# Kernel tuning notes

Hardware: AMD Instinct MI355X
Metric: run time of the kernel (lower is better)

The kernel has to match this reference:

```python
import jax, jax.numpy as jnp
import numpy as np

N_NODES = 50000
N_EDGES = 400000
NODE_FEAT = 32
HIDDEN = 256
ACTION_DIM = 6
NUM_GRAPHS = 64


def setup_inputs() -> dict:
    key = jax.random.key(0)
    ks = jax.random.split(key, 9)
    x = jax.random.normal(ks[0], (N_NODES, NODE_FEAT), dtype=jnp.float32)
    edge_index = jax.random.randint(ks[1], (2, N_EDGES), 0, N_NODES, dtype=jnp.int32)
    batch = jnp.sort(jax.random.randint(ks[2], (N_NODES,), 0, NUM_GRAPHS, dtype=jnp.int32))
    # GCNConv weights (PyG stores Linear without bias + separate bias term;
    # here W is [in, out] so h = x @ W)
    s1 = 1.0 / np.sqrt(NODE_FEAT)
    s2 = 1.0 / np.sqrt(HIDDEN)
    W1 = jax.random.uniform(ks[3], (NODE_FEAT, HIDDEN), jnp.float32, -s1, s1)
    b1 = jnp.zeros((HIDDEN,), jnp.float32)
    W2 = jax.random.uniform(ks[4], (HIDDEN, HIDDEN), jnp.float32, -s2, s2)
    b2 = jnp.zeros((HIDDEN,), jnp.float32)
    Wf = jax.random.uniform(ks[5], (HIDDEN, 2 * ACTION_DIM), jnp.float32, -s2, s2)
    bf = jax.random.uniform(ks[6], (2 * ACTION_DIM,), jnp.float32, -s2, s2)
    return {"x": x, "edge_index": edge_index, "batch": batch,
            "W1": W1, "b1": b1, "W2": W2, "b2": b2, "Wf": Wf, "bf": bf}


def gcn_conv(x, src, dst, deg_inv_sqrt, W, b, num_nodes):
    # PyG GCNConv: h = x @ W, messages h[src] * norm scattered to dst, + bias.
    h = x @ W  # [N, out]
    norm = deg_inv_sqrt[src] * deg_inv_sqrt[dst]  # [E+N]
    msgs = h[src] * norm[:, None]  # [E+N, out]  (dominant memory traffic)
    out = jax.ops.segment_sum(msgs, dst, num_segments=num_nodes)
    return out + b


def reference(x, edge_index, batch, W1, b1, W2, b2, Wf, bf):
    num_nodes = x.shape[0]
    loop = jnp.arange(num_nodes, dtype=edge_index.dtype)
    src = jnp.concatenate([edge_index[0], loop])  # self-loops, PyG default
    dst = jnp.concatenate([edge_index[1], loop])
    deg = jax.ops.segment_sum(jnp.ones_like(dst, dtype=x.dtype), dst,
                              num_segments=num_nodes)  # >=1 due to self-loops
    deg_inv_sqrt = jax.lax.rsqrt(deg)

    h = jax.nn.relu(gcn_conv(x, src, dst, deg_inv_sqrt, W1, b1, num_nodes))
    h = jax.nn.relu(gcn_conv(h, src, dst, deg_inv_sqrt, W2, b2, num_nodes))

    # global_mean_pool over graph ids
    sums = jax.ops.segment_sum(h, batch, num_segments=NUM_GRAPHS)
    counts = jax.ops.segment_sum(jnp.ones((num_nodes,), x.dtype), batch,
                                 num_segments=NUM_GRAPHS)
    pooled = sums / jnp.maximum(counts, 1.0)[:, None]  # [G, HIDDEN]

    mls = pooled @ Wf + bf  # [G, 2*ACTION_DIM]
    mean, log_std = jnp.split(mls, 2, axis=-1)
    std = jnp.exp(jnp.clip(log_std, -20.0, 2.0))
    return mean, std
```

## Files before the change

### kernel.cpp

```cpp
#include <hip/hip_runtime.h>
#include <math.h>

#define NN 50000
#define FEAT 32
#define HID 256
#define NGRAPH 64
#define CAP 48

typedef __attribute__((ext_vector_type(8))) short bfrag;
typedef __attribute__((ext_vector_type(8))) unsigned short u16x8;
typedef __attribute__((ext_vector_type(4))) float f32x4;

__device__ __forceinline__ float bf2f(unsigned short u) {
    union { unsigned int i; float f; } v; v.i = ((unsigned int)u) << 16; return v.f;
}
__device__ __forceinline__ unsigned short f2bf(float f) {
    union { float f; unsigned int i; } v; v.f = f;
    unsigned int r = v.i + 0x7fffu + ((v.i >> 16) & 1u);
    return (unsigned short)(r >> 16);
}

__device__ __forceinline__ void pack_w(const float* __restrict__ W,
                                       unsigned short* __restrict__ Wp, int K, int o) {
    int j    = o & 7;
    int lane = (o >> 3) & 63;
    int rest = o >> 9;
    int nst  = K >> 5;
    int ks   = rest & (nst - 1);
    int nb   = rest / nst;
    int n = nb * 16 + (lane & 15);
    int k = ks * 32 + (lane >> 4) * 8 + j;
    Wp[o] = f2bf(W[(size_t)k * HID + n]);
}

__global__ void k_prep(float4* __restrict__ zp, int n16) {
    int i = blockIdx.x * blockDim.x + threadIdx.x;
    if (i < n16) zp[i] = make_float4(0.f, 0.f, 0.f, 0.f);
}

__global__ void k_setup(const int* __restrict__ src, const int* __restrict__ dst,
                        const int* __restrict__ batch,
                        const float* __restrict__ W1, const float* __restrict__ W2,
                        int* __restrict__ counter, unsigned short* __restrict__ csr,
                        int* __restrict__ starts, float* __restrict__ pooled,
                        unsigned short* __restrict__ W1p, unsigned short* __restrict__ W2p,
                        int E, int N) {
    int e = blockIdx.x * blockDim.x + threadIdx.x;
    if (e < E) {
        int d = dst[e];
        int p = atomicAdd(&counter[d], 1);
        if (p < CAP) csr[(size_t)d * CAP + p] = (unsigned short)src[e];
    }
    if (e < N) {
        int b = batch[e];
        int prev = (e == 0) ? -1 : batch[e - 1];
        if (b != prev) {
            for (int g = prev + 1; g <= b; ++g) starts[g] = e;
        }
        if (e == N - 1) {
            for (int g = b + 1; g <= NGRAPH; ++g) starts[g] = N;
        }
    }
    if (e < FEAT * HID) pack_w(W1, W1p, FEAT, e);
    int o2 = e - FEAT * HID;
    if (o2 >= 0 && o2 < HID * HID) pack_w(W2, W2p, HID, o2);
    if (e < NGRAPH * HID) pooled[e] = 0.f;
}

__global__ void k_aggx(const float* __restrict__ x, const int* __restrict__ cnt,
                       const unsigned short* __restrict__ csr,
                       unsigned short* __restrict__ out, int N) {
    int node = blockIdx.x * 8 + (threadIdx.x >> 5);
    if (node >= N) return;
    int col = threadIdx.x & 31;
    int ecnt = cnt[node];
    float dn = rsqrtf((float)(ecnt + 1));
    int e = ecnt > CAP ? CAP : ecnt;
    const unsigned short* lst = &csr[(size_t)node * CAP];

    float acc = x[(size_t)node * FEAT + col] * dn;
    int i = 0;
    for (; i + 8 <= e; i += 8) {
        u16x8 s = *(const u16x8*)&lst[i];
        float vs[8];
#pragma unroll
        for (int j = 0; j < 8; ++j) {
            int sj = (int)s[j];
            vs[j] = x[(size_t)sj * FEAT + col] * rsqrtf((float)(cnt[sj] + 1));
        }
        acc += ((vs[0] + vs[1]) + (vs[2] + vs[3])) + ((vs[4] + vs[5]) + (vs[6] + vs[7]));
    }
    for (; i + 4 <= e; i += 4) {
        float vs[4];
#pragma unroll
        for (int j = 0; j < 4; ++j) {
            int sj = (int)lst[i + j];
            vs[j] = x[(size_t)sj * FEAT + col] * rsqrtf((float)(cnt[sj] + 1));
        }
        acc += (vs[0] + vs[1]) + (vs[2] + vs[3]);
    }
    for (; i < e; ++i) {
        int sj = (int)lst[i];
        acc += x[(size_t)sj * FEAT + col] * rsqrtf((float)(cnt[sj] + 1));
    }
    out[(size_t)node * FEAT + col] = f2bf(acc * dn);
}

__global__ void k_aggh(const unsigned short* __restrict__ hp, const int* __restrict__ cnt,
                       const unsigned short* __restrict__ csr,
                       unsigned short* __restrict__ outp, int N) {
    int panel = blockIdx.x & 7;
    int node = (blockIdx.x >> 3) * 64 + (threadIdx.x >> 2);
    if (node >= N) return;
    int c0 = (threadIdx.x & 3) * 8;
    const unsigned short* h = hp + (size_t)panel * N * 32;
    unsigned short* out = outp + (size_t)panel * N * 32;

    int ecnt = cnt[node];
    float dn = rsqrtf((float)(ecnt + 1));
    int e = ecnt > CAP ? CAP : ecnt;
    const unsigned short* lst = &csr[(size_t)node * CAP];

    bfrag sv = *(const bfrag*)&h[(size_t)node * 32 + c0];
    float a[8];
#pragma unroll
    for (int j = 0; j < 8; ++j) a[j] = bf2f((unsigned short)sv[j]);

    int i = 0;
    for (; i + 8 <= e; i += 8) {
        u16x8 s = *(const u16x8*)&lst[i];
        bfrag w0 = *(const bfrag*)&h[(size_t)s[0] * 32 + c0];
        bfrag w1 = *(const bfrag*)&h[(size_t)s[1] * 32 + c0];
        bfrag w2 = *(const bfrag*)&h[(size_t)s[2] * 32 + c0];
        bfrag w3 = *(const bfrag*)&h[(size_t)s[3] * 32 + c0];
        bfrag w4 = *(const bfrag*)&h[(size_t)s[4] * 32 + c0];
        bfrag w5 = *(const bfrag*)&h[(size_t)s[5] * 32 + c0];
        bfrag w6 = *(const bfrag*)&h[(size_t)s[6] * 32 + c0];
        bfrag w7 = *(const bfrag*)&h[(size_t)s[7] * 32 + c0];
#pragma unroll
        for (int j = 0; j < 8; ++j) {
            a[j] += ((bf2f((unsigned short)w0[j]) + bf2f((unsigned short)w1[j]))
                   + (bf2f((unsigned short)w2[j]) + bf2f((unsigned short)w3[j])))
                  + ((bf2f((unsigned short)w4[j]) + bf2f((unsigned short)w5[j]))
                   + (bf2f((unsigned short)w6[j]) + bf2f((unsigned short)w7[j])));
        }
    }
    for (; i + 4 <= e; i += 4) {
        bfrag w0 = *(const bfrag*)&h[(size_t)lst[i]     * 32 + c0];
        bfrag w1 = *(const bfrag*)&h[(size_t)lst[i + 1] * 32 + c0];
        bfrag w2 = *(const bfrag*)&h[(size_t)lst[i + 2] * 32 + c0];
        bfrag w3 = *(const bfrag*)&h[(size_t)lst[i + 3] * 32 + c0];
#pragma unroll
        for (int j = 0; j < 8; ++j)
            a[j] += (bf2f((unsigned short)w0[j]) + bf2f((unsigned short)w1[j]))
                  + (bf2f((unsigned short)w2[j]) + bf2f((unsigned short)w3[j]));
    }
    for (; i < e; ++i) {
        bfrag w = *(const bfrag*)&h[(size_t)lst[i] * 32 + c0];
#pragma unroll
        for (int j = 0; j < 8; ++j) a[j] += bf2f((unsigned short)w[j]);
    }
    bfrag o;
#pragma unroll
    for (int j = 0; j < 8; ++j) o[j] = (short)f2bf(a[j] * dn);
    *(bfrag*)&out[(size_t)node * 32 + c0] = o;
}

__global__ __launch_bounds__(256, 4)
void k_mmf(const unsigned short* __restrict__ A, const unsigned short* __restrict__ Wp,
           const float* __restrict__ bias, const int* __restrict__ cnt,
           unsigned short* __restrict__ C, int M) {
    __shared__ unsigned short lds[64 * 264];
    const int K = FEAT;
    int tid  = threadIdx.x;
    int lane = tid & 63;
    int wid  = tid >> 6;
    int l15  = lane & 15;
    int lq   = lane >> 4;
    int row0 = blockIdx.x * 64;

    const int P = K + 8;
    {
        int flat = tid * 8;
        int row = flat >> 5;
        int col = flat & 31;
        bfrag v = {0, 0, 0, 0, 0, 0, 0, 0};
        int gr = row0 + row;
        if (gr < M) v = *(const bfrag*)&A[(size_t)gr * K + col];
        *(bfrag*)&lds[row * P + col] = v;
    }
    __syncthreads();

    f32x4 acc[4][4];
#pragma unroll
    for (int mi = 0; mi < 4; ++mi)
#pragma unroll
        for (int ni = 0; ni < 4; ++ni) acc[mi][ni] = (f32x4){0.f, 0.f, 0.f, 0.f};

    bfrag fb[4];
#pragma unroll
    for (int ni = 0; ni < 4; ++ni) {
        size_t off = (((size_t)(wid * 4 + ni)) * 64 + lane) * 8;
        fb[ni] = *(const bfrag*)&Wp[off];
    }
    bfrag fa[4];
#pragma unroll
    for (int mi = 0; mi < 4; ++mi)
        fa[mi] = *(const bfrag*)&lds[(mi * 16 + l15) * P + lq * 8];
#pragma unroll
    for (int mi = 0; mi < 4; ++mi)
#pragma unroll
        for (int ni = 0; ni < 4; ++ni)
            acc[mi][ni] = __builtin_amdgcn_mfma_f32_16x16x32_bf16(fb[ni], fa[mi], acc[mi][ni], 0, 0, 0);

    float4 bv[4];
#pragma unroll
    for (int ni = 0; ni < 4; ++ni)
        bv[ni] = *(const float4*)&bias[(wid * 4 + ni) * 16 + lq * 4];
    float sv[4];
#pragma unroll
    for (int mi = 0; mi < 4; ++mi) {
        int gr = row0 + mi * 16 + l15;
        sv[mi] = (gr < M) ? rsqrtf((float)(cnt[gr] + 1)) : 0.f;
    }

    __syncthreads();
#pragma unroll
    for (int mi = 0; mi < 4; ++mi) {
#pragma unroll
        for (int ni = 0; ni < 4; ++ni) {
            const float* bp = (const float*)&bv[ni];
            ushort4 o;
            o.x = f2bf(fmaxf(acc[mi][ni][0] + bp[0], 0.f) * sv[mi]);
            o.y = f2bf(fmaxf(acc[mi][ni][1] + bp[1], 0.f) * sv[mi]);
            o.z = f2bf(fmaxf(acc[mi][ni][2] + bp[2], 0.f) * sv[mi]);
            o.w = f2bf(fmaxf(acc[mi][ni][3] + bp[3], 0.f) * sv[mi]);
            *(ushort4*)&lds[(mi * 16 + l15) * 264 + (wid * 4 + ni) * 16 + lq * 4] = o;
        }
    }
    __syncthreads();

#pragma unroll
    for (int i = 0; i < 8; ++i) {
        int F = (i * 256 + tid) * 8;
        int row = F >> 8;
        int col = F & 255;
        int gr = row0 + row;
        if (gr < M) {
            bfrag v = *(const bfrag*)&lds[row * 264 + col];
            *(bfrag*)&C[((size_t)(col >> 5) * M + gr) * 32 + (col & 31)] = v;
        }
    }
}

__global__ __launch_bounds__(256, 4)
void k_mmfp(const unsigned short* __restrict__ A, const unsigned short* __restrict__ Wp,
            const float* __restrict__ bias, const int* __restrict__ batch,
            float* __restrict__ pooled, int M) {
    __shared__ unsigned short lds[64 * 264];
    __shared__ int bshare[64];
    const int K = HID;
    int tid  = threadIdx.x;
    int lane = tid & 63;
    int wid  = tid >> 6;
    int l15  = lane & 15;
    int lq   = lane >> 4;
    int row0 = blockIdx.x * 64;

    if (tid < 64) {
        int gr = row0 + tid;
        bshare[tid] = (gr < M) ? batch[gr] : -1;
    }

    const int P = K + 8;
    for (int it = 0; it < 8; ++it) {
        int flat = (it * 256 + tid) * 8;
        int row = flat >> 8;
        int col = flat & 255;
        bfrag v = {0, 0, 0, 0, 0, 0, 0, 0};
        int gr = row0 + row;
        if (gr < M) v = *(const bfrag*)&A[((size_t)(col >> 5) * M + gr) * 32 + (col & 31)];
        *(bfrag*)&lds[row * P + col] = v;
    }
    __syncthreads();

    f32x4 acc[4][4];
#pragma unroll
    for (int mi = 0; mi < 4; ++mi)
#pragma unroll
        for (int ni = 0; ni < 4; ++ni) acc[mi][ni] = (f32x4){0.f, 0.f, 0.f, 0.f};

    for (int ks = 0; ks < 8; ++ks) {
        bfrag fb[4];
#pragma unroll
        for (int ni = 0; ni < 4; ++ni) {
            size_t off = (((size_t)(wid * 4 + ni) * 8 + ks) * 64 + lane) * 8;
            fb[ni] = *(const bfrag*)&Wp[off];
        }
        bfrag fa[4];
        int koff = ks * 32 + lq * 8;
#pragma unroll
        for (int mi = 0; mi < 4; ++mi)
            fa[mi] = *(const bfrag*)&lds[(mi * 16 + l15) * P + koff];
#pragma unroll
        for (int mi = 0; mi < 4; ++mi)
#pragma unroll
            for (int ni = 0; ni < 4; ++ni)
                acc[mi][ni] = __builtin_amdgcn_mfma_f32_16x16x32_bf16(fb[ni], fa[mi], acc[mi][ni], 0, 0, 0);
    }

    float4 bv[4];
#pragma unroll
    for (int ni = 0; ni < 4; ++ni)
        bv[ni] = *(const float4*)&bias[(wid * 4 + ni) * 16 + lq * 4];

    __syncthreads();
#pragma unroll
    for (int mi = 0; mi < 4; ++mi) {
#pragma unroll
        for (int ni = 0; ni < 4; ++ni) {
            const float* bp = (const float*)&bv[ni];
            ushort4 o;
            o.x = f2bf(fmaxf(acc[mi][ni][0] + bp[0], 0.f));
            o.y = f2bf(fmaxf(acc[mi][ni][1] + bp[1], 0.f));
            o.z = f2bf(fmaxf(acc[mi][ni][2] + bp[2], 0.f));
            o.w = f2bf(fmaxf(acc[mi][ni][3] + bp[3], 0.f));
            *(ushort4*)&lds[(mi * 16 + l15) * 264 + (wid * 4 + ni) * 16 + lq * 4] = o;
        }
    }
    __syncthreads();

    int c = tid;
    float pacc = 0.f;
    int cur = bshare[0];
    for (int r = 0; r < 64; ++r) {
        int g = bshare[r];
        if (g != cur) {
            if (cur >= 0) atomicAdd(&pooled[(size_t)cur * HID + c], pacc);
            pacc = 0.f; cur = g;
        }
        pacc += bf2f(lds[r * 264 + c]);
    }
    if (cur >= 0) atomicAdd(&pooled[(size_t)cur * HID + c], pacc);
}

__global__ void k_head(const float* __restrict__ pooled, const int* __restrict__ starts,
                       const float* __restrict__ Wf, const float* __restrict__ bf,
                       float* __restrict__ out) {
    int t = blockIdx.x * blockDim.x + threadIdx.x;
    if (t >= NGRAPH * 12) return;
    int g = t / 12, j = t % 12;
    float cntf = (float)(starts[g + 1] - starts[g]);
    float inv = 1.f / fmaxf(cntf, 1.f);
    float s = 0.f;
    for (int k = 0; k < HID; ++k) s += pooled[(size_t)g * HID + k] * Wf[k * 12 + j];
    s = s * inv + bf[j];
    if (j < 6) {
        out[g * 6 + j] = s;
    } else {
        float ls = fminf(fmaxf(s, -20.f), 2.f);
        out[NGRAPH * 6 + g * 6 + (j - 6)] = expf(ls);
    }
}

extern "C" void kernel_launch(void* const* d_in, const int* in_sizes, int n_in,
                              void* d_out, int out_size, void* d_ws, size_t ws_size,
                              hipStream_t stream) {
    const float* x     = (const float*)d_in[0];
    const int*   ei    = (const int*)d_in[1];
    const int*   batch = (const int*)d_in[2];
    const float* W1    = (const float*)d_in[3];
    const float* b1    = (const float*)d_in[4];
    const float* W2    = (const float*)d_in[5];
    const float* b2    = (const float*)d_in[6];
    const float* Wf    = (const float*)d_in[7];
    const float* bfv   = (const float*)d_in[8];
    float* out = (float*)d_out;

    const int E = in_sizes[1] / 2;
    const int N = in_sizes[2];
    const int* srcp = ei;
    const int* dstp = ei + E;

    char* ws = (char*)d_ws;
    const size_t OFF_CTR    = 0;
    const size_t OFF_POOLED = 200192;
    const size_t OFF_STARTS = 265728;
    const size_t OFF_W1P    = 266240;
    const size_t OFF_W2P    = 282624;
    const size_t OFF_CSR    = 413696;
    const size_t OFF_AGGX   = 5213696;
    const size_t OFF_H1     = 8413696;
    const size_t OFF_G      = 34013696;

    int*            ctr    = (int*)(ws + OFF_CTR);
    float*          pooled = (float*)(ws + OFF_POOLED);
    int*            starts = (int*)(ws + OFF_STARTS);
    unsigned short* W1p    = (unsigned short*)(ws + OFF_W1P);
    unsigned short* W2p    = (unsigned short*)(ws + OFF_W2P);
    unsigned short* csr    = (unsigned short*)(ws + OFF_CSR);
    unsigned short* aggX   = (unsigned short*)(ws + OFF_AGGX);
    unsigned short* h1     = (unsigned short*)(ws + OFF_H1);
    unsigned short* g      = (unsigned short*)(ws + OFF_G);

    const int T = 256;
    k_prep<<<(200192 / 16 + T - 1) / T, T, 0, stream>>>((float4*)ws, 200192 / 16);
    k_setup<<<(E + T - 1) / T, T, 0, stream>>>(srcp, dstp, batch, W1, W2,
                                               ctr, csr, starts, pooled, W1p, W2p, E, N);

    k_aggx<<<(N + 7) / 8, T, 0, stream>>>(x, ctr, csr, aggX, N);
    k_mmf<<<(N + 63) / 64, T, 0, stream>>>(aggX, W1p, b1, ctr, h1, N);

    k_aggh<<<((N + 63) / 64) * 8, T, 0, stream>>>(h1, ctr, csr, g, N);
    k_mmfp<<<(N + 63) / 64, T, 0, stream>>>(g, W2p, b2, batch, pooled, N);

    k_head<<<3, T, 0, stream>>>(pooled, starts, Wf, bfv, out);
}
```

Before: 118.5 us.

## Sort nodes by degree for aggregation and pre-scale x to bf16

Adds a kernel that writes x pre-multiplied by each node's inverse-sqrt degree in bf16 and builds a degree histogram. A second kernel builds a degree-sorted node permutation. Both aggregation kernels then walk nodes in that order so wavefronts see similar neighbour counts, which cuts divergence. The first-layer gather also drops the per-neighbour rsqrt and count load and reads half the bytes. The cost is two extra launches with atomics, scattered output writes from the permuted order, and bf16 rounding of the input features.

```diff
diff --git a/kernel.cpp b/kernel.cpp
--- a/kernel.cpp
+++ b/kernel.cpp
@@ -67,51 +67,81 @@
     if (e < NGRAPH * HID) pooled[e] = 0.f;
 }
 
-__global__ void k_aggx(const float* __restrict__ x, const int* __restrict__ cnt,
-                       const unsigned short* __restrict__ csr,
+__global__ void k_histx(const float* __restrict__ x, const int* __restrict__ cnt,
+                        unsigned short* __restrict__ xbf, int* __restrict__ hist, int N) {
+    __shared__ int lh[49];
+    if (threadIdx.x < 49) lh[threadIdx.x] = 0;
+    __syncthreads();
+    int node = blockIdx.x * 8 + (threadIdx.x >> 5);
+    int col = threadIdx.x & 31;
+    if (node < N) {
+        int ecnt = cnt[node];
+        float dn = rsqrtf((float)(ecnt + 1));
+        xbf[(size_t)node * FEAT + col] = f2bf(x[(size_t)node * FEAT + col] * dn);
+        if (col == 0) {
+            int e = ecnt > CAP ? CAP : ecnt;
+            atomicAdd(&lh[e], 1);
+        }
+    }
+    __syncthreads();
+    if (threadIdx.x < 49 && lh[threadIdx.x]) atomicAdd(&hist[threadIdx.x], lh[threadIdx.x]);
+}
+
+__global__ void k_perm(const int* __restrict__ cnt, const int* __restrict__ hist,
+                       int* __restrict__ cursor, int* __restrict__ perm, int N) {
+    __shared__ int pref[49];
+    if (threadIdx.x == 0) {
+        int s = 0;
+        for (int b = 0; b < 49; ++b) { pref[b] = s; s += hist[b]; }
+    }
+    __syncthreads();
+    int n = blockIdx.x * blockDim.x + threadIdx.x;
+    if (n < N) {
+        int e = cnt[n]; if (e > CAP) e = CAP;
+        int r = atomicAdd(&cursor[e], 1);
+        perm[pref[e] + r] = n;
+    }
+}
+
+__global__ void k_aggx(const unsigned short* __restrict__ xbf, const int* __restrict__ cnt,
+                       const unsigned short* __restrict__ csr, const int* __restrict__ perm,
                        unsigned short* __restrict__ out, int N) {
-    int node = blockIdx.x * 8 + (threadIdx.x >> 5);
-    if (node >= N) return;
+    int slot = blockIdx.x * 8 + (threadIdx.x >> 5);
+    if (slot >= N) return;
+    int node = perm[slot];
     int col = threadIdx.x & 31;
     int ecnt = cnt[node];
     float dn = rsqrtf((float)(ecnt + 1));
     int e = ecnt > CAP ? CAP : ecnt;
     const unsigned short* lst = &csr[(size_t)node * CAP];
 
-    float acc = x[(size_t)node * FEAT + col] * dn;
+    float acc = bf2f(xbf[(size_t)node * FEAT + col]);
     int i = 0;
     for (; i + 8 <= e; i += 8) {
         u16x8 s = *(const u16x8*)&lst[i];
         float vs[8];
 #pragma unroll
-        for (int j = 0; j < 8; ++j) {
-            int sj = (int)s[j];
-            vs[j] = x[(size_t)sj * FEAT + col] * rsqrtf((float)(cnt[sj] + 1));
-        }
+        for (int j = 0; j < 8; ++j) vs[j] = bf2f(xbf[(size_t)s[j] * FEAT + col]);
         acc += ((vs[0] + vs[1]) + (vs[2] + vs[3])) + ((vs[4] + vs[5]) + (vs[6] + vs[7]));
     }
     for (; i + 4 <= e; i += 4) {
-        float vs[4];
-#pragma unroll
-        for (int j = 0; j < 4; ++j) {
-            int sj = (int)lst[i + j];
-            vs[j] = x[(size_t)sj * FEAT + col] * rsqrtf((float)(cnt[sj] + 1));
-        }
-        acc += (vs[0] + vs[1]) + (vs[2] + vs[3]);
-    }
-    for (; i < e; ++i) {
-        int sj = (int)lst[i];
-        acc += x[(size_t)sj * FEAT + col] * rsqrtf((float)(cnt[sj] + 1));
-    }
+        float v0 = bf2f(xbf[(size_t)lst[i]     * FEAT + col]);
+        float v1 = bf2f(xbf[(size_t)lst[i + 1] * FEAT + col]);
+        float v2 = bf2f(xbf[(size_t)lst[i + 2] * FEAT + col]);
+        float v3 = bf2f(xbf[(size_t)lst[i + 3] * FEAT + col]);
+        acc += (v0 + v1) + (v2 + v3);
+    }
+    for (; i < e; ++i) acc += bf2f(xbf[(size_t)lst[i] * FEAT + col]);
     out[(size_t)node * FEAT + col] = f2bf(acc * dn);
 }
 
 __global__ void k_aggh(const unsigned short* __restrict__ hp, const int* __restrict__ cnt,
-                       const unsigned short* __restrict__ csr,
+                       const unsigned short* __restrict__ csr, const int* __restrict__ perm,
                        unsigned short* __restrict__ outp, int N) {
     int panel = blockIdx.x & 7;
-    int node = (blockIdx.x >> 3) * 64 + (threadIdx.x >> 2);
-    if (node >= N) return;
+    int slot = (blockIdx.x >> 3) * 64 + (threadIdx.x >> 2);
+    if (slot >= N) return;
+    int node = perm[slot];
     int c0 = (threadIdx.x & 3) * 8;
     const unsigned short* h = hp + (size_t)panel * N * 32;
     unsigned short* out = outp + (size_t)panel * N * 32;
@@ -384,34 +414,45 @@
 
     char* ws = (char*)d_ws;
     const size_t OFF_CTR    = 0;
-    const size_t OFF_POOLED = 200192;
-    const size_t OFF_STARTS = 265728;
-    const size_t OFF_W1P    = 266240;
-    const size_t OFF_W2P    = 282624;
-    const size_t OFF_CSR    = 413696;
-    const size_t OFF_AGGX   = 5213696;
-    const size_t OFF_H1     = 8413696;
-    const size_t OFF_G      = 34013696;
+    const size_t OFF_HIST   = 200192;
+    const size_t OFF_CURSOR = 200448;
+    const size_t ZERO_BYTES = 200704;
+    const size_t OFF_POOLED = 200704;
+    const size_t OFF_STARTS = 266240;
+    const size_t OFF_W1P    = 266752;
+    const size_t OFF_W2P    = 283136;
+    const size_t OFF_PERM   = 414208;
+    const size_t OFF_CSR    = 614400;
+    const size_t OFF_XBF    = 5414400;
+    const size_t OFF_AGGX   = 8614400;
+    const size_t OFF_H1     = 11814400;
+    const size_t OFF_G      = 37414400;
 
     int*            ctr    = (int*)(ws + OFF_CTR);
+    int*            hist   = (int*)(ws + OFF_HIST);
+    int*            cursor = (int*)(ws + OFF_CURSOR);
     float*          pooled = (float*)(ws + OFF_POOLED);
     int*            starts = (int*)(ws + OFF_STARTS);
     unsigned short* W1p    = (unsigned short*)(ws + OFF_W1P);
     unsigned short* W2p    = (unsigned short*)(ws + OFF_W2P);
+    int*            perm   = (int*)(ws + OFF_PERM);
     unsigned short* csr    = (unsigned short*)(ws + OFF_CSR);
+    unsigned short* xbf    = (unsigned short*)(ws + OFF_XBF);
     unsigned short* aggX   = (unsigned short*)(ws + OFF_AGGX);
     unsigned short* h1     = (unsigned short*)(ws + OFF_H1);
     unsigned short* g      = (unsigned short*)(ws + OFF_G);
 
     const int T = 256;
-    k_prep<<<(200192 / 16 + T - 1) / T, T, 0, stream>>>((float4*)ws, 200192 / 16);
+    k_prep<<<(ZERO_BYTES / 16 + T - 1) / T, T, 0, stream>>>((float4*)ws, ZERO_BYTES / 16);
     k_setup<<<(E + T - 1) / T, T, 0, stream>>>(srcp, dstp, batch, W1, W2,
                                                ctr, csr, starts, pooled, W1p, W2p, E, N);
-
-    k_aggx<<<(N + 7) / 8, T, 0, stream>>>(x, ctr, csr, aggX, N);
+    k_histx<<<(N + 7) / 8, T, 0, stream>>>(x, ctr, xbf, hist, N);
+    k_perm<<<(N + T - 1) / T, T, 0, stream>>>(ctr, hist, cursor, perm, N);
+
+    k_aggx<<<(N + 7) / 8, T, 0, stream>>>(xbf, ctr, csr, perm, aggX, N);
     k_mmf<<<(N + 63) / 64, T, 0, stream>>>(aggX, W1p, b1, ctr, h1, N);
 
-    k_aggh<<<((N + 63) / 64) * 8, T, 0, stream>>>(h1, ctr, csr, g, N);
+    k_aggh<<<((N + 63) / 64) * 8, T, 0, stream>>>(h1, ctr, csr, perm, g, N);
     k_mmfp<<<(N + 63) / 64, T, 0, stream>>>(g, W2p, b2, batch, pooled, N);
 
     k_head<<<3, T, 0, stream>>>(pooled, starts, Wf, bfv, out);
```

After: 365.4 us. 3.08x slower.
